# Kernel optimization log

Measured on AMD Instinct MI355X. Metric: run time of the kernel, lower is better.

## Reference

```python
import jax, jax.numpy as jnp
import numpy as np
from jax import lax

# dims
B, T = 64, 1024
ANNOT, RNN, MEM, ATTN = 512, 1024, 512, 512
FILTERS, KSIZE = 32, 31
PAD = (KSIZE - 1) // 2  # 15, SAME padding


def setup_inputs() -> dict:
    key = jax.random.key(0)
    ks = jax.random.split(key, 20)
    s = 0.02
    return {
        "memory": jax.random.normal(ks[0], (B, MEM), jnp.float32),
        "context": jax.random.normal(ks[1], (B, ANNOT), jnp.float32),
        "rnn_state": jax.random.normal(ks[2], (B, RNN), jnp.float32),
        "annots": jax.random.normal(ks[3], (B, T, ANNOT), jnp.float32),
        "atten": jax.random.uniform(ks[4], (B, 2, T), jnp.float32),
        "mask": jnp.ones((B, T), jnp.int32),
        "t": 0,
        # GRUCell params (torch gate order: r, z, n)
        "W_ih": jax.random.normal(ks[5], (3 * RNN, ANNOT + MEM), jnp.float32) * s,
        "W_hh": jax.random.normal(ks[6], (3 * RNN, RNN), jnp.float32) * s,
        "b_ih": jnp.zeros((3 * RNN,), jnp.float32),
        "b_hh": jnp.zeros((3 * RNN,), jnp.float32),
        # location-sensitive attention params
        "conv_w": jax.random.normal(ks[7], (FILTERS, 2, KSIZE), jnp.float32) * s,
        "loc_w": jax.random.normal(ks[8], (ATTN, FILTERS), jnp.float32) * s,
        "loc_b": jnp.zeros((ATTN,), jnp.float32),
        "q_w": jax.random.normal(ks[9], (ATTN, RNN), jnp.float32) * s,
        "q_b": jnp.zeros((ATTN,), jnp.float32),
        "a_w": jax.random.normal(ks[10], (ATTN, ANNOT), jnp.float32) * s,
        "a_b": jnp.zeros((ATTN,), jnp.float32),
        "v_w": jax.random.normal(ks[11], (1, ATTN), jnp.float32) * s,
    }


def _gru_cell(x, h, W_ih, W_hh, b_ih, b_hh):
    gi = x @ W_ih.T + b_ih  # [B, 3H]
    gh = h @ W_hh.T + b_hh
    i_r, i_z, i_n = jnp.split(gi, 3, axis=-1)
    h_r, h_z, h_n = jnp.split(gh, 3, axis=-1)
    r = jax.nn.sigmoid(i_r + h_r)
    z = jax.nn.sigmoid(i_z + h_z)
    n = jnp.tanh(i_n + r * h_n)
    return (1.0 - z) * n + z * h


def reference(memory, context, rnn_state, annots, atten, mask, t,
              W_ih, W_hh, b_ih, b_hh, conv_w, loc_w, loc_b,
              q_w, q_b, a_w, a_b, v_w):
    # GRU step on [memory; prev_context]
    rnn_input = jnp.concatenate([memory, context], axis=-1)  # [B, MEM+ANNOT]
    rnn_output = _gru_cell(rnn_input, rnn_state, W_ih, W_hh, b_ih, b_hh)  # [B, RNN]

    # location features: SAME conv over [B, 2, T] -> [B, FILTERS, T]
    loc_conv = lax.conv_general_dilated(
        atten, conv_w, window_strides=(1,), padding=[(PAD, PAD)],
        dimension_numbers=("NCH", "OIH", "NCH"))
    processed_loc = jnp.einsum("bft,af->bta", loc_conv, loc_w) + loc_b  # [B,T,ATTN]

    processed_query = (rnn_output @ q_w.T + q_b)[:, None, :]            # [B,1,ATTN]
    processed_annots = jnp.einsum("btd,ad->bta", annots, a_w) + a_b     # [B,T,ATTN]

    energy = jnp.tanh(processed_query + processed_annots + processed_loc)
    alignment = jnp.einsum("bta,a->bt", energy, v_w[0])                 # [B,T]

    # mask fill with -inf where mask == 0
    alignment = jnp.where(mask == 0, -jnp.inf, alignment)

    # sigmoid-normalized attention weights
    sig = jax.nn.sigmoid(alignment)
    alignment = sig / jnp.sum(sig, axis=1, keepdims=True)               # [B,T]

    new_context = jnp.einsum("bt,btd->bd", alignment, annots)           # [B,ANNOT]
    return rnn_output, new_context, alignment
```

## Files before the change

kernel.cpp:

```cpp
#include <hip/hip_runtime.h>

typedef float f32x4 __attribute__((ext_vector_type(4)));
typedef short bf16x8 __attribute__((ext_vector_type(8)));

__device__ __forceinline__ unsigned int pk2(float a, float b) {
    unsigned int ua = __float_as_uint(a); ua += 0x7FFFu + ((ua >> 16) & 1u);
    unsigned int ub = __float_as_uint(b); ub += 0x7FFFu + ((ub >> 16) & 1u);
    return __builtin_amdgcn_perm(ub, ua, 0x07060302u);
}
__device__ __forceinline__ unsigned short bf16_rne(float a) {
    unsigned int ua = __float_as_uint(a);
    ua += 0x7FFFu + ((ua >> 16) & 1u);
    return (unsigned short)(ua >> 16);
}
__device__ __forceinline__ float tanh_fast(float x) {
    float e = __expf(x + x);
    return 1.f - 2.f / (e + 1.f);
}
__device__ __forceinline__ f32x4 mfma16(bf16x8 a, bf16x8 b, f32x4 c) {
    return __builtin_amdgcn_mfma_f32_16x16x32_bf16(a, b, c, 0, 0, 0);
}
__device__ __forceinline__ void ald16(const void* g, void* l) {
    __builtin_amdgcn_global_load_lds(
        (const __attribute__((address_space(1))) unsigned int*)g,
        (__attribute__((address_space(3))) unsigned int*)l, 16, 0, 0);
}

#define Q_WIH   786432
#define Q_WHH   1572864
#define Q_QW    1703936
#define Q_X2    1720320
#define Q_X1    1736704
#define Q_BAW   1802240
#define Q_BLW   1806336
#define Q_EB    1806464
#define NCVT    7057

__global__ __launch_bounds__(256) void k_prep(
    const float* __restrict__ Wih, const float* __restrict__ Whh,
    const float* __restrict__ qw, const float* __restrict__ rnn_state,
    const float* __restrict__ memory, const float* __restrict__ context,
    const float* __restrict__ aw, const float* __restrict__ lw,
    const float* __restrict__ ab, const float* __restrict__ lb,
    const float* __restrict__ atten, const float* __restrict__ convw,
    unsigned short* __restrict__ Wihb, unsigned short* __restrict__ Whhb,
    unsigned short* __restrict__ qwb, unsigned short* __restrict__ X2b,
    unsigned short* __restrict__ X1b, unsigned short* __restrict__ Bbig,
    float* __restrict__ ebias, unsigned short* __restrict__ Lconv)
{
    __shared__ float att_s[2 * 160];
    __shared__ float cw_s[1984];
    const int tid = threadIdx.x;
    if (blockIdx.x < NCVT) {
        int q = blockIdx.x * 256 + tid;
        if (q >= Q_EB) return;
        if (q < Q_WIH) {
            int i = q * 4;
            float4 v = *(const float4*)(Wih + i);
            uint2 u; u.x = pk2(v.x, v.y); u.y = pk2(v.z, v.w);
            *(uint2*)(Wihb + i) = u;
        } else if (q < Q_WHH) {
            int i = (q - Q_WIH) * 4;
            float4 v = *(const float4*)(Whh + i);
            uint2 u; u.x = pk2(v.x, v.y); u.y = pk2(v.z, v.w);
            *(uint2*)(Whhb + i) = u;
        } else if (q < Q_QW) {
            int i = (q - Q_WHH) * 4;
            float4 v = *(const float4*)(qw + i);
            uint2 u; u.x = pk2(v.x, v.y); u.y = pk2(v.z, v.w);
            *(uint2*)(qwb + i) = u;
        } else if (q < Q_X2) {
            int i = (q - Q_QW) * 4;
            float4 v = *(const float4*)(rnn_state + i);
            uint2 u; u.x = pk2(v.x, v.y); u.y = pk2(v.z, v.w);
            *(uint2*)(X2b + i) = u;
        } else if (q < Q_X1) {
            int i = (q - Q_X2) * 4;
            int b = i >> 10, c = i & 1023;
            const float* s = (c < 512) ? (memory + b * 512 + c) : (context + b * 512 + (c - 512));
            float4 v = *(const float4*)s;
            uint2 u; u.x = pk2(v.x, v.y); u.y = pk2(v.z, v.w);
            *(uint2*)(X1b + i) = u;
        } else if (q < Q_BAW) {
            int i = (q - Q_X1) * 4;
            int a = i >> 9, c = i & 511;
            float4 v = *(const float4*)(aw + a * 512 + c);
            uint2 u; u.x = pk2(v.x, v.y); u.y = pk2(v.z, v.w);
            *(uint2*)(Bbig + a * 544 + c) = u;
        } else if (q < Q_BLW) {
            int i = (q - Q_BAW) * 4;
            int a = i >> 5, c = i & 31;
            float4 v = *(const float4*)(lw + a * 32 + c);
            uint2 u; u.x = pk2(v.x, v.y); u.y = pk2(v.z, v.w);
            *(uint2*)(Bbig + a * 544 + 512 + c) = u;
        } else {
            int i = (q - Q_BLW) * 4;
            float4 va = *(const float4*)(ab + i);
            float4 vb = *(const float4*)(lb + i);
            float4 r; r.x = va.x + vb.x; r.y = va.y + vb.y; r.z = va.z + vb.z; r.w = va.w + vb.w;
            *(float4*)(ebias + i) = r;
        }
    } else {
        const int bid = blockIdx.x - NCVT;
        const int b = bid >> 3;
        const int tbase = (bid & 7) * 128;
        for (int i = tid; i < 320; i += 256) {
            int c = i / 160, j = i % 160;
            float v = 0.f;
            int pos = tbase - 15 + j;
            if (j < 158 && pos >= 0 && pos < 1024) v = atten[b * 2048 + c * 1024 + pos];
            att_s[c * 160 + j] = v;
        }
        for (int i = tid; i < 1984; i += 256) cw_s[i] = convw[i];
        __syncthreads();
        const int f = tid & 31, tq = tid >> 5;
        float acc[16];
#pragma unroll
        for (int i = 0; i < 16; ++i) acc[i] = 0.f;
        for (int c = 0; c < 2; ++c) {
            for (int k = 0; k < 31; ++k) {
                float w = cw_s[f * 62 + c * 31 + k];
                int base = c * 160 + tq * 16 + k;
#pragma unroll
                for (int ti = 0; ti < 16; ++ti) acc[ti] += w * att_s[base + ti];
            }
        }
#pragma unroll
        for (int ti = 0; ti < 16; ++ti) {
            int t = tbase + tq * 16 + ti;
            Lconv[(b * 1024 + t) * 32 + f] = bf16_rne(acc[ti]);
        }
    }
}

__global__ __launch_bounds__(256, 4) void k_gemm_ks(
    const unsigned short* __restrict__ A1, const unsigned short* __restrict__ A2,
    const unsigned short* __restrict__ B1, const unsigned short* __restrict__ B2,
    float* __restrict__ C, int N, int nTiles, int n_split, int K, int Klen)
{
    __shared__ __align__(16) unsigned short As[64 * 32];
    __shared__ __align__(16) unsigned short Bs[128 * 32];
    const int tid = threadIdx.x;
    const int nb = blockIdx.x % nTiles;
    const int ks = blockIdx.x / nTiles;
    const int nBase = nb * 128;
    const bool use2 = nBase >= n_split;
    const unsigned short* A = use2 ? A2 : A1;
    const unsigned short* B = use2 ? B2 : B1;
    const int brow0 = nBase - (use2 ? n_split : 0);
    const int lane = tid & 63, w = tid >> 6;
    const int c = lane & 15, qd = lane >> 4;
    const int lr = lane >> 2;
    const int swzl = ((lane & 3) ^ ((lr >> 1) & 3)) * 8;

    const f32x4 fz = {0.f, 0.f, 0.f, 0.f};
    f32x4 acc[4][2];
#pragma unroll
    for (int i = 0; i < 4; ++i) { acc[i][0] = fz; acc[i][1] = fz; }

    const int k0b = ks * Klen;
    const int nkc = Klen >> 5;
    for (int kc = 0; kc < nkc; ++kc) {
        const int k0 = k0b + kc * 32;
        ald16(A + (size_t)(w * 16 + lr) * K + k0 + swzl, &As[w * 512]);
        ald16(B + (size_t)(brow0 + w * 16 + lr) * K + k0 + swzl, &Bs[w * 512]);
        ald16(B + (size_t)(brow0 + 64 + w * 16 + lr) * K + k0 + swzl, &Bs[2048 + w * 512]);
        __syncthreads();
        const int rdoff = (qd ^ ((c >> 1) & 3)) * 8;
        bf16x8 af[4];
#pragma unroll
        for (int i = 0; i < 4; ++i) af[i] = *(const bf16x8*)&As[(i * 16 + c) * 32 + rdoff];
#pragma unroll
        for (int j = 0; j < 2; ++j) {
            bf16x8 bj = *(const bf16x8*)&Bs[(w * 32 + j * 16 + c) * 32 + rdoff];
#pragma unroll
            for (int i = 0; i < 4; ++i) acc[i][j] = mfma16(af[i], bj, acc[i][j]);
        }
        __syncthreads();
    }
    float* Cp = C + (size_t)ks * 64 * N;
#pragma unroll
    for (int i = 0; i < 4; ++i)
#pragma unroll
        for (int r = 0; r < 4; ++r) {
            int row = i * 16 + qd * 4 + r;
#pragma unroll
            for (int j = 0; j < 2; ++j) {
                int col = nBase + w * 32 + j * 16 + c;
                Cp[row * N + col] = acc[i][j][r];
            }
        }
}

__global__ __launch_bounds__(256) void k_gates(
    const float* __restrict__ Cg, const float* __restrict__ h0,
    const float* __restrict__ bih, const float* __restrict__ bhh,
    float* __restrict__ outv, unsigned short* __restrict__ X3b)
{
    int idx = blockIdx.x * 256 + threadIdx.x;
    int b = idx >> 10, h = idx & 1023;
    const float* g0 = Cg + b * 6144;
    const float* g1 = Cg + 393216 + b * 6144;
    float ir = g0[h] + g1[h] + bih[h];
    float iz = g0[h + 1024] + g1[h + 1024] + bih[h + 1024];
    float inn = g0[h + 2048] + g1[h + 2048] + bih[h + 2048];
    float hr = g0[h + 3072] + g1[h + 3072] + bhh[h];
    float hz = g0[h + 4096] + g1[h + 4096] + bhh[h + 1024];
    float hn = g0[h + 5120] + g1[h + 5120] + bhh[h + 2048];
    float r = 1.f / (1.f + __expf(-(ir + hr)));
    float z = 1.f / (1.f + __expf(-(iz + hz)));
    float n = tanh_fast(inn + r * hn);
    float o = (1.f - z) * n + z * h0[idx];
    outv[idx] = o;
    X3b[idx] = bf16_rne(o);
}

__global__ __launch_bounds__(256, 2) void k_attn(
    const float* __restrict__ annots, const unsigned short* __restrict__ Lconv,
    const unsigned short* __restrict__ Bbig, const float* __restrict__ pqP,
    const float* __restrict__ qb, const float* __restrict__ ebias,
    const float* __restrict__ vw, float* __restrict__ wsal)
{
    __shared__ __align__(16) unsigned short As[2][64 * 32];
    __shared__ __align__(16) unsigned short Bs[2][512 * 32];
    __shared__ float red[4][64];
    const int tid = threadIdx.x;
    const int btBase = blockIdx.x * 64;
    const int b = btBase >> 10;
    const int lane = tid & 63, w = tid >> 6;
    const int c = lane & 15, qd = lane >> 4;
    const int lr = lane >> 2;
    const int swzl = ((lane & 3) ^ ((lr >> 1) & 3)) * 8;
    const int arow = tid >> 2, alc = tid & 3;
    const int apofs = (alc ^ ((arow >> 1) & 3)) * 8;

    const f32x4 fz = {0.f, 0.f, 0.f, 0.f};
    f32x4 acc[4][8];
#pragma unroll
    for (int i = 0; i < 4; ++i)
#pragma unroll
        for (int j = 0; j < 8; ++j) acc[i][j] = fz;

    const float* aP = annots + (size_t)(btBase + arow) * 512 + alc * 8;
    const unsigned short* bP = Bbig + (size_t)(w * 16 + lr) * 544 + swzl;

#pragma unroll
    for (int s = 0; s < 8; ++s)
        ald16(bP + (size_t)s * 64 * 544, &Bs[0][s * 2048 + w * 512]);
    {
        float4 v0 = *(const float4*)(aP);
        float4 v1 = *(const float4*)(aP + 4);
        uint4 u;
        u.x = pk2(v0.x, v0.y); u.y = pk2(v0.z, v0.w);
        u.z = pk2(v1.x, v1.y); u.w = pk2(v1.z, v1.w);
        *(uint4*)&As[0][arow * 32 + apofs] = u;
    }
    __syncthreads();

    for (int kc = 0; kc < 17; ++kc) {
        const int cur = kc & 1, nxt = cur ^ 1;
        float4 v0n, v1n;
        if (kc < 16) {
            const int k1 = (kc + 1) * 32;
#pragma unroll
            for (int s = 0; s < 8; ++s)
                ald16(bP + (size_t)s * 64 * 544 + k1, &Bs[nxt][s * 2048 + w * 512]);
            if (kc < 15) {
                v0n = *(const float4*)(aP + k1);
                v1n = *(const float4*)(aP + k1 + 4);
            } else {
                ald16(Lconv + (size_t)(btBase + w * 16 + lr) * 32 + swzl, &As[nxt][w * 512]);
            }
        }
        const int rdoff = (qd ^ ((c >> 1) & 3)) * 8;
        bf16x8 af[4];
#pragma unroll
        for (int i = 0; i < 4; ++i) af[i] = *(const bf16x8*)&As[cur][(i * 16 + c) * 32 + rdoff];
        __builtin_amdgcn_s_setprio(1);
#pragma unroll
        for (int j = 0; j < 8; ++j) {
            bf16x8 bj = *(const bf16x8*)&Bs[cur][(w * 128 + j * 16 + c) * 32 + rdoff];
#pragma unroll
            for (int i = 0; i < 4; ++i) acc[i][j] = mfma16(af[i], bj, acc[i][j]);
        }
        __builtin_amdgcn_s_setprio(0);
        if (kc < 16) {
            if (kc < 15) {
                uint4 u;
                u.x = pk2(v0n.x, v0n.y); u.y = pk2(v0n.z, v0n.w);
                u.z = pk2(v1n.x, v1n.y); u.w = pk2(v1n.z, v1n.w);
                *(uint4*)&As[nxt][arow * 32 + apofs] = u;
            }
            __syncthreads();
        }
    }
    float pe[8], vv[8];
#pragma unroll
    for (int j = 0; j < 8; ++j) {
        int colg = w * 128 + j * 16 + c;
        pe[j] = pqP[b * 512 + colg] + pqP[32768 + b * 512 + colg] + qb[colg] + ebias[colg];
        vv[j] = vw[colg];
    }
#pragma unroll
    for (int i = 0; i < 4; ++i)
#pragma unroll
        for (int r = 0; r < 4; ++r) {
            float p = 0.f;
#pragma unroll
            for (int j = 0; j < 8; ++j)
                p += vv[j] * tanh_fast(acc[i][j][r] + pe[j]);
            p += __shfl_xor(p, 1);
            p += __shfl_xor(p, 2);
            p += __shfl_xor(p, 4);
            p += __shfl_xor(p, 8);
            if (c == 0) red[w][i * 16 + qd * 4 + r] = p;
        }
    __syncthreads();
    if (tid < 64)
        wsal[btBase + tid] = red[0][tid] + red[1][tid] + red[2][tid] + red[3][tid];
}

__global__ __launch_bounds__(256) void k_ctx(
    const float* __restrict__ annots, const float* __restrict__ wsal,
    const int* __restrict__ mask, float* __restrict__ out)
{
    __shared__ float al[1024];
    __shared__ float wsum[4];
    __shared__ float red[256];
    const int b = blockIdx.x >> 3;
    const int chunk = blockIdx.x & 7;
    const int tid = threadIdx.x;
    float lsum = 0.f;
#pragma unroll
    for (int p = 0; p < 4; ++p) {
        int t = p * 256 + tid;
        int bt = b * 1024 + t;
        float raw = wsal[bt];
        float s = (mask[bt] != 0) ? 1.f / (1.f + __expf(-raw)) : 0.f;
        al[t] = s;
        lsum += s;
    }
    for (int off = 32; off > 0; off >>= 1) lsum += __shfl_xor(lsum, off);
    if ((tid & 63) == 0) wsum[tid >> 6] = lsum;
    __syncthreads();
    const float tot = wsum[0] + wsum[1] + wsum[2] + wsum[3];
    const float inv = 1.f / tot;
    if (chunk == 0) {
#pragma unroll
        for (int p = 0; p < 4; ++p) {
            int t = p * 256 + tid;
            out[98304 + b * 1024 + t] = al[t] * inv;
        }
    }
    const int dq = tid & 63, tq = tid >> 6;
    const int d = chunk * 64 + dq;
    const float* ap = annots + (size_t)(b * 1024 + tq * 256) * 512 + d;
    float acc = 0.f;
#pragma unroll 4
    for (int t = 0; t < 256; ++t) acc += al[tq * 256 + t] * ap[(size_t)t * 512];
    red[tid] = acc;
    __syncthreads();
    if (tid < 64) {
        float s2 = red[tid] + red[64 + tid] + red[128 + tid] + red[192 + tid];
        out[65536 + b * 512 + chunk * 64 + tid] = s2 * inv;
    }
}

extern "C" void kernel_launch(void* const* d_in, const int* in_sizes, int n_in,
                              void* d_out, int out_size, void* d_ws, size_t ws_size,
                              hipStream_t stream) {
    const float* memory    = (const float*)d_in[0];
    const float* context   = (const float*)d_in[1];
    const float* rnn_state = (const float*)d_in[2];
    const float* annots    = (const float*)d_in[3];
    const float* atten     = (const float*)d_in[4];
    const int*   mask      = (const int*)d_in[5];
    const float* W_ih   = (const float*)d_in[7];
    const float* W_hh   = (const float*)d_in[8];
    const float* b_ih   = (const float*)d_in[9];
    const float* b_hh   = (const float*)d_in[10];
    const float* conv_w = (const float*)d_in[11];
    const float* loc_w  = (const float*)d_in[12];
    const float* loc_b  = (const float*)d_in[13];
    const float* q_w    = (const float*)d_in[14];
    const float* q_b    = (const float*)d_in[15];
    const float* a_w    = (const float*)d_in[16];
    const float* a_b    = (const float*)d_in[17];
    const float* v_w    = (const float*)d_in[18];
    float* out = (float*)d_out;

    char* w8 = (char*)d_ws;
    unsigned short* Lconv = (unsigned short*)(w8 + 0);
    unsigned short* Bbig  = (unsigned short*)(w8 + 4194304);
    unsigned short* Wihb  = (unsigned short*)(w8 + 4751360);
    unsigned short* Whhb  = (unsigned short*)(w8 + 11042816);
    unsigned short* qwb   = (unsigned short*)(w8 + 17334272);
    unsigned short* X1b   = (unsigned short*)(w8 + 18382848);
    unsigned short* X2b   = (unsigned short*)(w8 + 18513920);
    unsigned short* X3b   = (unsigned short*)(w8 + 18644992);
    float*          Cgru  = (float*)(w8 + 18776064);
    float*          pqP   = (float*)(w8 + 18776064);
    float*          wsal  = (float*)(w8 + 19038208);
    float*          ebias = (float*)(w8 + 21921792);

    k_prep<<<NCVT + 512, 256, 0, stream>>>(W_ih, W_hh, q_w, rnn_state, memory, context,
                                           a_w, loc_w, a_b, loc_b, atten, conv_w,
                                           Wihb, Whhb, qwb, X2b, X1b, Bbig, ebias, Lconv);
    k_gemm_ks<<<96, 256, 0, stream>>>(X1b, X2b, Wihb, Whhb, Cgru, 6144, 48, 3072, 1024, 512);
    k_gates<<<256, 256, 0, stream>>>(Cgru, rnn_state, b_ih, b_hh, out, X3b);
    k_gemm_ks<<<8, 256, 0, stream>>>(X3b, X3b, qwb, qwb, pqP, 512, 4, 0x40000000, 1024, 512);
    k_attn<<<1024, 256, 0, stream>>>(annots, Lconv, Bbig, pqP, q_b, ebias, v_w, wsal);
    k_ctx<<<512, 256, 0, stream>>>(annots, wsal, mask, out);
}
```

Before: 342.9 us.

## Deepen annots prefetch, split-K query GEMM wider, split context into partial+reduce kernels

The attention kernel now prefetches annotation rows two K-chunks ahead in registers, so global load latency is hidden behind more MFMA work. The query-projection GEMM launches 32 blocks with a smaller K-split, giving 8 partial sums that k_attn adds up. The context reduction becomes two kernels. k_ctxA does coalesced float4 time-chunked partial sums and writes them to a workspace, then k_ctxB normalizes and reduces them. This trades an extra launch and workspace traffic for better memory access patterns and parallelism.

After: 346.4 us. Within noise of the previous version (+1.0%).

```diff
diff --git a/kernel.cpp b/kernel.cpp
--- a/kernel.cpp
+++ b/kernel.cpp
@@ -233,6 +233,7 @@
     const int swzl = ((lane & 3) ^ ((lr >> 1) & 3)) * 8;
     const int arow = tid >> 2, alc = tid & 3;
     const int apofs = (alc ^ ((arow >> 1) & 3)) * 8;
+    const int rdoff = (qd ^ ((c >> 1) & 3)) * 8;
 
     const f32x4 fz = {0.f, 0.f, 0.f, 0.f};
     f32x4 acc[4][8];
@@ -255,24 +256,25 @@
         u.z = pk2(v1.x, v1.y); u.w = pk2(v1.z, v1.w);
         *(uint4*)&As[0][arow * 32 + apofs] = u;
     }
+    float4 avC0 = *(const float4*)(aP + 32);
+    float4 avC1 = *(const float4*)(aP + 36);
     __syncthreads();
 
     for (int kc = 0; kc < 17; ++kc) {
         const int cur = kc & 1, nxt = cur ^ 1;
-        float4 v0n, v1n;
+        float4 f0, f1;
+        if (kc <= 13) {
+            f0 = *(const float4*)(aP + (kc + 2) * 32);
+            f1 = *(const float4*)(aP + (kc + 2) * 32 + 4);
+        }
         if (kc < 16) {
             const int k1 = (kc + 1) * 32;
 #pragma unroll
             for (int s = 0; s < 8; ++s)
                 ald16(bP + (size_t)s * 64 * 544 + k1, &Bs[nxt][s * 2048 + w * 512]);
-            if (kc < 15) {
-                v0n = *(const float4*)(aP + k1);
-                v1n = *(const float4*)(aP + k1 + 4);
-            } else {
+            if (kc == 15)
                 ald16(Lconv + (size_t)(btBase + w * 16 + lr) * 32 + swzl, &As[nxt][w * 512]);
-            }
-        }
-        const int rdoff = (qd ^ ((c >> 1) & 3)) * 8;
+        }
         bf16x8 af[4];
 #pragma unroll
         for (int i = 0; i < 4; ++i) af[i] = *(const bf16x8*)&As[cur][(i * 16 + c) * 32 + rdoff];
@@ -284,21 +286,23 @@
             for (int i = 0; i < 4; ++i) acc[i][j] = mfma16(af[i], bj, acc[i][j]);
         }
         __builtin_amdgcn_s_setprio(0);
-        if (kc < 16) {
-            if (kc < 15) {
-                uint4 u;
-                u.x = pk2(v0n.x, v0n.y); u.y = pk2(v0n.z, v0n.w);
-                u.z = pk2(v1n.x, v1n.y); u.w = pk2(v1n.z, v1n.w);
-                *(uint4*)&As[nxt][arow * 32 + apofs] = u;
-            }
-            __syncthreads();
-        }
+        if (kc <= 14) {
+            uint4 u;
+            u.x = pk2(avC0.x, avC0.y); u.y = pk2(avC0.z, avC0.w);
+            u.z = pk2(avC1.x, avC1.y); u.w = pk2(avC1.z, avC1.w);
+            *(uint4*)&As[nxt][arow * 32 + apofs] = u;
+        }
+        if (kc <= 13) { avC0 = f0; avC1 = f1; }
+        if (kc < 16) __syncthreads();
     }
     float pe[8], vv[8];
 #pragma unroll
     for (int j = 0; j < 8; ++j) {
         int colg = w * 128 + j * 16 + c;
-        pe[j] = pqP[b * 512 + colg] + pqP[32768 + b * 512 + colg] + qb[colg] + ebias[colg];
+        float s = qb[colg] + ebias[colg];
+#pragma unroll
+        for (int p = 0; p < 8; ++p) s += pqP[p * 32768 + b * 512 + colg];
+        pe[j] = s;
         vv[j] = vw[colg];
     }
 #pragma unroll
@@ -320,15 +324,48 @@
         wsal[btBase + tid] = red[0][tid] + red[1][tid] + red[2][tid] + red[3][tid];
 }
 
-__global__ __launch_bounds__(256) void k_ctx(
+__global__ __launch_bounds__(256) void k_ctxA(
     const float* __restrict__ annots, const float* __restrict__ wsal,
-    const int* __restrict__ mask, float* __restrict__ out)
-{
-    __shared__ float al[1024];
+    const int* __restrict__ mask, float* __restrict__ ctxP)
+{
+    __shared__ float cx[4][512];
+    const int b = blockIdx.x >> 3;
+    const int tc = blockIdx.x & 7;
+    const int tid = threadIdx.x, lane = tid & 63, wv = tid >> 6;
+    const int t0 = tc * 128 + wv * 32;
+    const float* wp = wsal + b * 1024;
+    const int* mp = mask + b * 1024;
+    const float* ap = annots + (size_t)(b * 1024 + t0) * 512 + lane * 4;
+
+    float a0 = 0.f, a1 = 0.f, a2 = 0.f, a3 = 0.f;
+    float a4 = 0.f, a5 = 0.f, a6 = 0.f, a7 = 0.f;
+#pragma unroll 4
+    for (int r = 0; r < 32; ++r) {
+        int t = t0 + r;
+        float raw = wp[t];
+        float s = (mp[t] != 0) ? 1.f / (1.f + __expf(-raw)) : 0.f;
+        float4 va = *(const float4*)(ap + (size_t)r * 512);
+        float4 vb = *(const float4*)(ap + (size_t)r * 512 + 256);
+        a0 += s * va.x; a1 += s * va.y; a2 += s * va.z; a3 += s * va.w;
+        a4 += s * vb.x; a5 += s * vb.y; a6 += s * vb.z; a7 += s * vb.w;
+    }
+    cx[wv][lane * 4 + 0] = a0; cx[wv][lane * 4 + 1] = a1;
+    cx[wv][lane * 4 + 2] = a2; cx[wv][lane * 4 + 3] = a3;
+    cx[wv][256 + lane * 4 + 0] = a4; cx[wv][256 + lane * 4 + 1] = a5;
+    cx[wv][256 + lane * 4 + 2] = a6; cx[wv][256 + lane * 4 + 3] = a7;
+    __syncthreads();
+    float* cp = ctxP + (size_t)(tc * 64 + b) * 512;
+    cp[tid]       = cx[0][tid]       + cx[1][tid]       + cx[2][tid]       + cx[3][tid];
+    cp[tid + 256] = cx[0][tid + 256] + cx[1][tid + 256] + cx[2][tid + 256] + cx[3][tid + 256];
+}
+
+__global__ __launch_bounds__(256) void k_ctxB(
+    const float* __restrict__ wsal, const int* __restrict__ mask,
+    const float* __restrict__ ctxP, float* __restrict__ out)
+{
+    __shared__ float sv[1024];
     __shared__ float wsum[4];
-    __shared__ float red[256];
-    const int b = blockIdx.x >> 3;
-    const int chunk = blockIdx.x & 7;
+    const int b = blockIdx.x;
     const int tid = threadIdx.x;
     float lsum = 0.f;
 #pragma unroll
@@ -337,7 +374,7 @@
         int bt = b * 1024 + t;
         float raw = wsal[bt];
         float s = (mask[bt] != 0) ? 1.f / (1.f + __expf(-raw)) : 0.f;
-        al[t] = s;
+        sv[t] = s;
         lsum += s;
     }
     for (int off = 32; off > 0; off >>= 1) lsum += __shfl_xor(lsum, off);
@@ -345,24 +382,19 @@
     __syncthreads();
     const float tot = wsum[0] + wsum[1] + wsum[2] + wsum[3];
     const float inv = 1.f / tot;
-    if (chunk == 0) {
-#pragma unroll
-        for (int p = 0; p < 4; ++p) {
-            int t = p * 256 + tid;
-            out[98304 + b * 1024 + t] = al[t] * inv;
-        }
-    }
-    const int dq = tid & 63, tq = tid >> 6;
-    const int d = chunk * 64 + dq;
-    const float* ap = annots + (size_t)(b * 1024 + tq * 256) * 512 + d;
-    float acc = 0.f;
-#pragma unroll 4
-    for (int t = 0; t < 256; ++t) acc += al[tq * 256 + t] * ap[(size_t)t * 512];
-    red[tid] = acc;
-    __syncthreads();
-    if (tid < 64) {
-        float s2 = red[tid] + red[64 + tid] + red[128 + tid] + red[192 + tid];
-        out[65536 + b * 512 + chunk * 64 + tid] = s2 * inv;
+#pragma unroll
+    for (int p = 0; p < 4; ++p) {
+        int t = p * 256 + tid;
+        out[98304 + b * 1024 + t] = sv[t] * inv;
+    }
+#pragma unroll
+    for (int h = 0; h < 2; ++h) {
+        int d = h * 256 + tid;
+        float csum = 0.f;
+#pragma unroll
+        for (int tc = 0; tc < 8; ++tc)
+            csum += ctxP[(size_t)(tc * 64 + b) * 512 + d];
+        out[65536 + b * 512 + d] = csum * inv;
     }
 }
 
@@ -400,7 +432,8 @@
     unsigned short* X3b   = (unsigned short*)(w8 + 18644992);
     float*          Cgru  = (float*)(w8 + 18776064);
     float*          pqP   = (float*)(w8 + 18776064);
-    float*          wsal  = (float*)(w8 + 19038208);
+    float*          ctxP  = (float*)(w8 + 18776064);
+    float*          wsal  = (float*)(w8 + 19824640);
     float*          ebias = (float*)(w8 + 21921792);
 
     k_prep<<<NCVT + 512, 256, 0, stream>>>(W_ih, W_hh, q_w, rnn_state, memory, context,
@@ -408,7 +441,8 @@
                                            Wihb, Whhb, qwb, X2b, X1b, Bbig, ebias, Lconv);
     k_gemm_ks<<<96, 256, 0, stream>>>(X1b, X2b, Wihb, Whhb, Cgru, 6144, 48, 3072, 1024, 512);
     k_gates<<<256, 256, 0, stream>>>(Cgru, rnn_state, b_ih, b_hh, out, X3b);
-    k_gemm_ks<<<8, 256, 0, stream>>>(X3b, X3b, qwb, qwb, pqP, 512, 4, 0x40000000, 1024, 512);
+    k_gemm_ks<<<32, 256, 0, stream>>>(X3b, X3b, qwb, qwb, pqP, 512, 4, 0x40000000, 1024, 128);
     k_attn<<<1024, 256, 0, stream>>>(annots, Lconv, Bbig, pqP, q_b, ebias, v_w, wsal);
-    k_ctx<<<512, 256, 0, stream>>>(annots, wsal, mask, out);
-}
+    k_ctxA<<<512, 256, 0, stream>>>(annots, wsal, mask, ctxP);
+    k_ctxB<<<64, 256, 0, stream>>>(wsal, mask, ctxP, out);
+}
```
